# Performance work log

Hardware: AMD Instinct MI355X
Metric: run time of the kernel (lower is better)

The kernel has to match this reference:

```python
import jax, jax.numpy as jnp
import numpy as np


def setup_inputs() -> dict:
    key = jax.random.key(0)
    k1, k2, k3, k4 = jax.random.split(key, 4)
    B, T_dec, T_enc, H2 = 8, 64, 512, 512  # H2 = 2*hiddenSize
    encoderOutput = jax.random.normal(k1, (B, T_enc, H2), dtype=jnp.float32)
    decoderInput = jax.random.normal(k2, (B, T_dec, H2), dtype=jnp.float32)
    # fc: Linear(4H -> 2H); torch weight layout [out, in] = [2H, 4H]
    W = jax.random.normal(k3, (H2, 2 * H2), dtype=jnp.float32) * (1.0 / np.sqrt(2 * H2))
    b = jax.random.normal(k4, (H2,), dtype=jnp.float32) * 0.01
    return {"encoderOutput": encoderOutput, "decoderInput": decoderInput, "W": W, "b": b}


def reference(encoderOutput, decoderInput, W, b):
    # Original: for each (i, j), fc(cat(dec[:,i], enc[:,j])) then log_softmax over
    # the FEATURE dim (dim=1 of the flattened [-1, 2H] tensor), then
    # context[:, i] = sum_j log_softmax(...) * enc[:, j].
    H2 = encoderOutput.shape[-1]
    W_dec = W[:, :H2]   # columns multiplying the decoder half of the concat
    W_enc = W[:, H2:]   # columns multiplying the encoder half
    dec_part = jnp.einsum('bid,od->bio', decoderInput, W_dec)   # [B, T_dec, 2H]
    enc_part = jnp.einsum('bjd,od->bjo', encoderOutput, W_enc)  # [B, T_enc, 2H]
    logits = dec_part[:, :, None, :] + enc_part[:, None, :, :] + b  # [B, T_dec, T_enc, 2H]
    alpha = jax.nn.log_softmax(logits, axis=-1)  # softmax over feature dim, as in source
    context = jnp.einsum('bijd,bjd->bid', alpha, encoderOutput)  # [B, T_dec, 2H]
    return context
```

## Files before the change

### kernel.cpp

```cpp
#include <hip/hip_runtime.h>


namespace {
constexpr int kH  = 512;
constexpr int kTD = 64;
constexpr int kTE = 512;
constexpr int kB  = 8;
constexpr int kRD = kB * kTD;
constexpr int kRE = kB * kTE;
constexpr int kRT = kRD + kRE;
}

typedef __attribute__((ext_vector_type(8))) short short8;
typedef __attribute__((ext_vector_type(4))) float floatx4;

__device__ __forceinline__ unsigned short f2bf(float x) {
    unsigned u = __float_as_uint(x);
    u += 0x7fffu + ((u >> 16) & 1u);
    return (unsigned short)(u >> 16);
}
__device__ __forceinline__ float bf2f(unsigned short h) {
    return __uint_as_float(((unsigned)h) << 16);
}

__global__ __launch_bounds__(256) void cast_misc(
    const float* __restrict__ W, const float* __restrict__ dec,
    unsigned short* __restrict__ Wd, unsigned short* __restrict__ We,
    unsigned short* __restrict__ dec_bf,
    float* __restrict__ S1, float* __restrict__ S2)
{
    const int idx = blockIdx.x * 256 + threadIdx.x;
    const int row = idx >> 10, col = idx & 1023;
    const unsigned short v = f2bf(W[idx]);
    if (col < kH) Wd[row * kH + col] = v;
    else          We[row * kH + (col - kH)] = v;
    if (idx < kRD * kH) dec_bf[idx] = f2bf(dec[idx]);
    if (idx < kB * kH) { S1[idx] = 0.f; S2[idx] = 0.f; }
}

__global__ __launch_bounds__(256) void cast_enc(
    const float* __restrict__ enc, unsigned short* __restrict__ enc_bf)
{
    const int idx = blockIdx.x * 256 + threadIdx.x;
    const float4 v = ((const float4*)enc)[idx];
    ushort4 o;
    o.x = f2bf(v.x); o.y = f2bf(v.y); o.z = f2bf(v.z); o.w = f2bf(v.w);
    ((ushort4*)enc_bf)[idx] = o;
}

__global__ __launch_bounds__(64) void gemm1(
    const unsigned short* __restrict__ enc_bf,
    const unsigned short* __restrict__ dec_bf,
    const unsigned short* __restrict__ Wd,
    const unsigned short* __restrict__ We,
    const float* __restrict__ bias,
    unsigned short* __restrict__ part_bf, unsigned short* __restrict__ uv)
{
    const int tile = blockIdx.x;
    const int ns = tile & 7, ms = tile >> 3;
    const int l = threadIdx.x;
    const int lr = l & 15, lq = l >> 4;
    const bool isenc = (ms >= 8);
    const unsigned short* A = isenc ? (enc_bf + (size_t)(ms - 8) * 64 * kH)
                                    : (dec_bf + (size_t)ms * 64 * kH);
    const unsigned short* Bw = isenc ? We : Wd;
    const unsigned short* a0 = A + (size_t)lr * kH + lq * 8;
    const unsigned short* b0 = Bw + (size_t)(ns * 64 + lr) * kH + lq * 8;

    floatx4 acc[4][4];
#pragma unroll
    for (int m = 0; m < 4; ++m)
#pragma unroll
        for (int n = 0; n < 4; ++n) acc[m][n] = (floatx4){0.f, 0.f, 0.f, 0.f};

    for (int k0 = 0; k0 < kH; k0 += 32) {
        short8 af[4], bf[4];
#pragma unroll
        for (int m = 0; m < 4; ++m) af[m] = *(const short8*)(a0 + (size_t)m * 16 * kH + k0);
#pragma unroll
        for (int n = 0; n < 4; ++n) bf[n] = *(const short8*)(b0 + (size_t)n * 16 * kH + k0);
#pragma unroll
        for (int m = 0; m < 4; ++m)
#pragma unroll
            for (int n = 0; n < 4; ++n)
                acc[m][n] = __builtin_amdgcn_mfma_f32_16x16x32_bf16(af[m], bf[n], acc[m][n], 0, 0, 0);
    }

    const int rowbase = ms * 64, colbase = ns * 64;
#pragma unroll
    for (int n = 0; n < 4; ++n) {
        const int col = colbase + n * 16 + lr;
        const float bv = isenc ? bias[col] : 0.f;
#pragma unroll
        for (int m = 0; m < 4; ++m) {
            const int row0 = rowbase + m * 16 + lq * 4;
#pragma unroll
            for (int r = 0; r < 4; ++r) {
                const float v = acc[m][n][r];
                const size_t off = (size_t)(row0 + r) * kH + col;
                part_bf[off] = f2bf(v);
                uv[off]      = f2bf(__expf(v + bv));
            }
        }
    }
}

__global__ __launch_bounds__(256) void transpose_enc(
    const float* __restrict__ enc, unsigned short* __restrict__ encT)
{
    __shared__ unsigned short s[32][33];
    const int b = blockIdx.z, j0 = blockIdx.y * 32, d0 = blockIdx.x * 32;
    const int tx = threadIdx.x & 31, ty = threadIdx.x >> 5;
    const float* src = enc + ((size_t)b * kTE + j0) * kH + d0;
#pragma unroll
    for (int jj = 0; jj < 32; jj += 8)
        s[ty + jj][tx] = f2bf(src[(size_t)(ty + jj) * kH + tx]);
    __syncthreads();
    unsigned short* dst = encT + ((size_t)b * kH + d0) * kTE + j0;
#pragma unroll
    for (int dd = 0; dd < 32; dd += 8)
        dst[(size_t)(ty + dd) * kTE + tx] = s[tx][ty + dd];
}

__global__ __launch_bounds__(256) void s1s2_k(
    const float* __restrict__ enc, const unsigned short* __restrict__ part_bf,
    float* __restrict__ S1, float* __restrict__ S2)
{
    const int d = blockIdx.x * 256 + threadIdx.x;
    const int b = blockIdx.y, jc = blockIdx.z;
    const float* e = enc + ((size_t)b * kTE + jc * 32) * kH + d;
    const unsigned short* p = part_bf + (size_t)(kRD + b * kTE + jc * 32) * kH + d;
    float s1 = 0.f, s2 = 0.f;
#pragma unroll 4
    for (int j = 0; j < 32; ++j) {
        const float ev = e[(size_t)j * kH];
        const float pv = bf2f(p[(size_t)j * kH]);
        s1 += ev;
        s2 = fmaf(pv, ev, s2);
    }
    atomicAdd(&S1[b * kH + d], s1);
    atomicAdd(&S2[b * kH + d], s2);
}

__global__ __launch_bounds__(64) void pgemm_lse(
    const unsigned short* __restrict__ uv, unsigned short* __restrict__ lse_bf)
{
    const int w = blockIdx.x;
    const int b = w >> 7, rem = w & 127;
    const int it = rem >> 5, jt = rem & 31;
    const int l = threadIdx.x;
    const int lr = l & 15, lq = l >> 4;
    const unsigned short* ua = uv + (size_t)(b * 64 + it * 16 + lr) * kH + lq * 8;
    const unsigned short* vb = uv + (size_t)(kRD + b * kTE + jt * 16 + lr) * kH + lq * 8;

    floatx4 acc = (floatx4){0.f, 0.f, 0.f, 0.f};
    for (int k0 = 0; k0 < kH; k0 += 32)
        acc = __builtin_amdgcn_mfma_f32_16x16x32_bf16(
            *(const short8*)(ua + k0), *(const short8*)(vb + k0), acc, 0, 0, 0);

    const int jcol = jt * 16 + lr;
#pragma unroll
    for (int r = 0; r < 4; ++r) {
        const int i = it * 16 + lq * 4 + r;
        lse_bf[(size_t)(b * kTD + i) * kTE + jcol] = f2bf(__logf(acc[r]));
    }
}

__global__ __launch_bounds__(64) void final_k(
    const unsigned short* __restrict__ lse_bf,
    const unsigned short* __restrict__ encT,
    const unsigned short* __restrict__ part_bf,
    const float* __restrict__ bias,
    const float* __restrict__ S1, const float* __restrict__ S2,
    float* __restrict__ out)
{
    const int w = blockIdx.x;
    const int b = w >> 7, rem = w & 127;
    const int it = rem >> 5, dt = rem & 31;
    const int l = threadIdx.x;
    const int lr = l & 15, lq = l >> 4;
    const unsigned short* la = lse_bf + (size_t)(b * kTD + it * 16 + lr) * kTE + lq * 8;
    const unsigned short* eb = encT + ((size_t)b * kH + dt * 16 + lr) * kTE + lq * 8;

    floatx4 acc = (floatx4){0.f, 0.f, 0.f, 0.f};
    for (int k0 = 0; k0 < kTE; k0 += 32)
        acc = __builtin_amdgcn_mfma_f32_16x16x32_bf16(
            *(const short8*)(la + k0), *(const short8*)(eb + k0), acc, 0, 0, 0);

    const int d = dt * 16 + lr;
    const float s1 = S1[b * kH + d], s2 = S2[b * kH + d], bv = bias[d];
#pragma unroll
    for (int r = 0; r < 4; ++r) {
        const int i = it * 16 + lq * 4 + r;
        const float dp = bf2f(part_bf[(size_t)(b * kTD + i) * kH + d]);
        out[(size_t)(b * kTD + i) * kH + d] = fmaf(dp + bv, s1, s2) - acc[r];
    }
}

extern "C" void kernel_launch(void* const* d_in, const int* in_sizes, int n_in,
                              void* d_out, int out_size, void* d_ws, size_t ws_size,
                              hipStream_t stream)
{
    (void)in_sizes; (void)n_in; (void)out_size; (void)ws_size;
    const float* enc  = (const float*)d_in[0];
    const float* dec  = (const float*)d_in[1];
    const float* W    = (const float*)d_in[2];
    const float* bias = (const float*)d_in[3];
    float* out = (float*)d_out;

    char* base = (char*)d_ws;
    unsigned short* part_bf = (unsigned short*)(base);
    unsigned short* uv      = (unsigned short*)(base + 4718592);
    unsigned short* encX    = (unsigned short*)(base + 9437184);
    unsigned short* dec_bf  = (unsigned short*)(base + 13631488);
    unsigned short* Wd      = (unsigned short*)(base + 14155776);
    unsigned short* We      = (unsigned short*)(base + 14680064);
    unsigned short* lse_bf  = (unsigned short*)(base + 15204352);
    float*          S1      = (float*)(base + 15728640);
    float*          S2      = (float*)(base + 15745024);

    cast_misc<<<2048, 256, 0, stream>>>(W, dec, Wd, We, dec_bf, S1, S2);
    cast_enc<<<2048, 256, 0, stream>>>(enc, encX);
    gemm1<<<576, 64, 0, stream>>>(encX, dec_bf, Wd, We, bias, part_bf, uv);
    transpose_enc<<<dim3(16, 16, 8), 256, 0, stream>>>(enc, encX);
    s1s2_k<<<dim3(2, 8, 16), 256, 0, stream>>>(enc, part_bf, S1, S2);
    pgemm_lse<<<1024, 64, 0, stream>>>(uv, lse_bf);
    final_k<<<1024, 64, 0, stream>>>(lse_bf, encX, part_bf, bias, S1, S2, out);
}
```

Measured before the change: 108.0 us.

## Fuse casts, transpose, and reductions; split-K GEMMs across four waves

Merges the weight/decoder cast, encoder cast and encoder transpose into one kernel, and merges the LSE pgemm with the S1/S2 reduction into one launch. This cuts the launch count from seven to four. gemm1 and the two small GEMMs move from single-wave 64-thread blocks to 256-thread blocks: gemm1 gives each wave a quadrant of the tile, while the LSE and final GEMMs split K across four waves and reduce through LDS with vectorized epilogues. The intent is fewer launches and better latency hiding per block. The cost is extra LDS reduction work, a __syncthreads per block, and fewer blocks in the final GEMM.

```diff
diff --git a/kernel.cpp b/kernel.cpp
--- a/kernel.cpp
+++ b/kernel.cpp
@@ -8,7 +8,6 @@
 constexpr int kB  = 8;
 constexpr int kRD = kB * kTD;
 constexpr int kRE = kB * kTE;
-constexpr int kRT = kRD + kRE;
 }
 
 typedef __attribute__((ext_vector_type(8))) short short8;
@@ -23,32 +22,46 @@
     return __uint_as_float(((unsigned)h) << 16);
 }
 
-__global__ __launch_bounds__(256) void cast_misc(
+__global__ __launch_bounds__(256) void fused_cast(
     const float* __restrict__ W, const float* __restrict__ dec,
+    const float* __restrict__ enc,
     unsigned short* __restrict__ Wd, unsigned short* __restrict__ We,
     unsigned short* __restrict__ dec_bf,
+    unsigned short* __restrict__ enc_bf, unsigned short* __restrict__ encT,
     float* __restrict__ S1, float* __restrict__ S2)
 {
-    const int idx = blockIdx.x * 256 + threadIdx.x;
-    const int row = idx >> 10, col = idx & 1023;
-    const unsigned short v = f2bf(W[idx]);
-    if (col < kH) Wd[row * kH + col] = v;
-    else          We[row * kH + (col - kH)] = v;
-    if (idx < kRD * kH) dec_bf[idx] = f2bf(dec[idx]);
-    if (idx < kB * kH) { S1[idx] = 0.f; S2[idx] = 0.f; }
-}
-
-__global__ __launch_bounds__(256) void cast_enc(
-    const float* __restrict__ enc, unsigned short* __restrict__ enc_bf)
-{
-    const int idx = blockIdx.x * 256 + threadIdx.x;
-    const float4 v = ((const float4*)enc)[idx];
-    ushort4 o;
-    o.x = f2bf(v.x); o.y = f2bf(v.y); o.z = f2bf(v.z); o.w = f2bf(v.w);
-    ((ushort4*)enc_bf)[idx] = o;
-}
-
-__global__ __launch_bounds__(64) void gemm1(
+    const int blk = blockIdx.x, t = threadIdx.x;
+    if (blk < 2048) {
+        const int idx = blk * 256 + t;
+        const int row = idx >> 10, col = idx & 1023;
+        const unsigned short v = f2bf(W[idx]);
+        if (col < kH) Wd[row * kH + col] = v;
+        else          We[row * kH + (col - kH)] = v;
+        if (idx < kRD * kH) dec_bf[idx] = f2bf(dec[idx]);
+        if (idx < kB * kH) { S1[idx] = 0.f; S2[idx] = 0.f; }
+    } else {
+        __shared__ unsigned short s[32][33];
+        const int tid = blk - 2048;
+        const int b = tid >> 8, rem = tid & 255;
+        const int j0 = (rem >> 4) * 32, d0 = (rem & 15) * 32;
+        const int tx = t & 31, ty = t >> 5;
+        const float* src = enc + ((size_t)b * kTE + j0) * kH + d0;
+        unsigned short* edst = enc_bf + ((size_t)b * kTE + j0) * kH + d0;
+#pragma unroll
+        for (int jj = 0; jj < 32; jj += 8) {
+            const unsigned short h = f2bf(src[(size_t)(ty + jj) * kH + tx]);
+            s[ty + jj][tx] = h;
+            edst[(size_t)(ty + jj) * kH + tx] = h;
+        }
+        __syncthreads();
+        unsigned short* tdst = encT + ((size_t)b * kH + d0) * kTE + j0;
+#pragma unroll
+        for (int dd = 0; dd < 32; dd += 8)
+            tdst[(size_t)(ty + dd) * kTE + tx] = s[tx][ty + dd];
+    }
+}
+
+__global__ __launch_bounds__(256) void gemm1(
     const unsigned short* __restrict__ enc_bf,
     const unsigned short* __restrict__ dec_bf,
     const unsigned short* __restrict__ Wd,
@@ -58,41 +71,42 @@
 {
     const int tile = blockIdx.x;
     const int ns = tile & 7, ms = tile >> 3;
-    const int l = threadIdx.x;
+    const int t = threadIdx.x, w = t >> 6, l = t & 63;
+    const int qm = w >> 1, qn = w & 1;
     const int lr = l & 15, lq = l >> 4;
     const bool isenc = (ms >= 8);
     const unsigned short* A = isenc ? (enc_bf + (size_t)(ms - 8) * 64 * kH)
                                     : (dec_bf + (size_t)ms * 64 * kH);
     const unsigned short* Bw = isenc ? We : Wd;
-    const unsigned short* a0 = A + (size_t)lr * kH + lq * 8;
-    const unsigned short* b0 = Bw + (size_t)(ns * 64 + lr) * kH + lq * 8;
-
-    floatx4 acc[4][4];
-#pragma unroll
-    for (int m = 0; m < 4; ++m)
-#pragma unroll
-        for (int n = 0; n < 4; ++n) acc[m][n] = (floatx4){0.f, 0.f, 0.f, 0.f};
+    const unsigned short* a0 = A + (size_t)(qm * 32 + lr) * kH + lq * 8;
+    const unsigned short* b0 = Bw + (size_t)(ns * 64 + qn * 32 + lr) * kH + lq * 8;
+
+    floatx4 acc[2][2];
+#pragma unroll
+    for (int m = 0; m < 2; ++m)
+#pragma unroll
+        for (int n = 0; n < 2; ++n) acc[m][n] = (floatx4){0.f, 0.f, 0.f, 0.f};
 
     for (int k0 = 0; k0 < kH; k0 += 32) {
-        short8 af[4], bf[4];
-#pragma unroll
-        for (int m = 0; m < 4; ++m) af[m] = *(const short8*)(a0 + (size_t)m * 16 * kH + k0);
-#pragma unroll
-        for (int n = 0; n < 4; ++n) bf[n] = *(const short8*)(b0 + (size_t)n * 16 * kH + k0);
-#pragma unroll
-        for (int m = 0; m < 4; ++m)
-#pragma unroll
-            for (int n = 0; n < 4; ++n)
+        short8 af[2], bf[2];
+#pragma unroll
+        for (int m = 0; m < 2; ++m) af[m] = *(const short8*)(a0 + (size_t)m * 16 * kH + k0);
+#pragma unroll
+        for (int n = 0; n < 2; ++n) bf[n] = *(const short8*)(b0 + (size_t)n * 16 * kH + k0);
+#pragma unroll
+        for (int m = 0; m < 2; ++m)
+#pragma unroll
+            for (int n = 0; n < 2; ++n)
                 acc[m][n] = __builtin_amdgcn_mfma_f32_16x16x32_bf16(af[m], bf[n], acc[m][n], 0, 0, 0);
     }
 
-    const int rowbase = ms * 64, colbase = ns * 64;
-#pragma unroll
-    for (int n = 0; n < 4; ++n) {
+    const int rowbase = ms * 64 + qm * 32, colbase = ns * 64 + qn * 32;
+#pragma unroll
+    for (int n = 0; n < 2; ++n) {
         const int col = colbase + n * 16 + lr;
         const float bv = isenc ? bias[col] : 0.f;
 #pragma unroll
-        for (int m = 0; m < 4; ++m) {
+        for (int m = 0; m < 2; ++m) {
             const int row0 = rowbase + m * 16 + lq * 4;
 #pragma unroll
             for (int r = 0; r < 4; ++r) {
@@ -105,68 +119,69 @@
     }
 }
 
-__global__ __launch_bounds__(256) void transpose_enc(
-    const float* __restrict__ enc, unsigned short* __restrict__ encT)
-{
-    __shared__ unsigned short s[32][33];
-    const int b = blockIdx.z, j0 = blockIdx.y * 32, d0 = blockIdx.x * 32;
-    const int tx = threadIdx.x & 31, ty = threadIdx.x >> 5;
-    const float* src = enc + ((size_t)b * kTE + j0) * kH + d0;
-#pragma unroll
-    for (int jj = 0; jj < 32; jj += 8)
-        s[ty + jj][tx] = f2bf(src[(size_t)(ty + jj) * kH + tx]);
-    __syncthreads();
-    unsigned short* dst = encT + ((size_t)b * kH + d0) * kTE + j0;
-#pragma unroll
-    for (int dd = 0; dd < 32; dd += 8)
-        dst[(size_t)(ty + dd) * kTE + tx] = s[tx][ty + dd];
-}
-
-__global__ __launch_bounds__(256) void s1s2_k(
+__global__ __launch_bounds__(256) void lse_s1s2(
+    const unsigned short* __restrict__ uv, unsigned short* __restrict__ lse_bf,
     const float* __restrict__ enc, const unsigned short* __restrict__ part_bf,
     float* __restrict__ S1, float* __restrict__ S2)
 {
-    const int d = blockIdx.x * 256 + threadIdx.x;
-    const int b = blockIdx.y, jc = blockIdx.z;
-    const float* e = enc + ((size_t)b * kTE + jc * 32) * kH + d;
-    const unsigned short* p = part_bf + (size_t)(kRD + b * kTE + jc * 32) * kH + d;
-    float s1 = 0.f, s2 = 0.f;
+    __shared__ float red[4][16][68];
+    const int blk = blockIdx.x, t = threadIdx.x;
+    if (blk < 256) {
+        const int b = blk >> 5, rem = blk & 31;
+        const int it = rem >> 3, jt = rem & 7;
+        const int w = t >> 6, l = t & 63;
+        const int lr = l & 15, lq = l >> 4;
+        const unsigned short* ua = uv + (size_t)(b * 64 + it * 16 + lr) * kH + w * 128 + lq * 8;
+        const unsigned short* vb = uv + (size_t)(kRD + b * kTE + jt * 64 + lr) * kH + w * 128 + lq * 8;
+
+        floatx4 acc[4];
+#pragma unroll
+        for (int n = 0; n < 4; ++n) acc[n] = (floatx4){0.f, 0.f, 0.f, 0.f};
+#pragma unroll
+        for (int k0 = 0; k0 < 128; k0 += 32) {
+            const short8 af = *(const short8*)(ua + k0);
+#pragma unroll
+            for (int n = 0; n < 4; ++n)
+                acc[n] = __builtin_amdgcn_mfma_f32_16x16x32_bf16(
+                    af, *(const short8*)(vb + (size_t)n * 16 * kH + k0), acc[n], 0, 0, 0);
+        }
+#pragma unroll
+        for (int n = 0; n < 4; ++n)
+#pragma unroll
+            for (int r = 0; r < 4; ++r)
+                red[w][lq * 4 + r][n * 16 + lr] = acc[n][r];
+        __syncthreads();
+        const int i = t >> 4, j0 = (t & 15) * 4;
+        float4 s = *(const float4*)&red[0][i][j0];
+        const float4 s1 = *(const float4*)&red[1][i][j0];
+        const float4 s2 = *(const float4*)&red[2][i][j0];
+        const float4 s3 = *(const float4*)&red[3][i][j0];
+        s.x += s1.x + s2.x + s3.x; s.y += s1.y + s2.y + s3.y;
+        s.z += s1.z + s2.z + s3.z; s.w += s1.w + s2.w + s3.w;
+        ushort4 o;
+        o.x = f2bf(__logf(s.x)); o.y = f2bf(__logf(s.y));
+        o.z = f2bf(__logf(s.z)); o.w = f2bf(__logf(s.w));
+        *(ushort4*)(lse_bf + (size_t)(b * kTD + it * 16 + i) * kTE + jt * 64 + j0) = o;
+    } else {
+        const int blk2 = blk - 256;
+        const int jc = blk2 & 15, b = (blk2 >> 4) & 7, dh = blk2 >> 7;
+        const int d = dh * 256 + t;
+        const float* e = enc + ((size_t)b * kTE + jc * 32) * kH + d;
+        const unsigned short* p = part_bf + (size_t)(kRD + b * kTE + jc * 32) * kH + d;
+        float s1 = 0.f, s2 = 0.f;
 #pragma unroll 4
-    for (int j = 0; j < 32; ++j) {
-        const float ev = e[(size_t)j * kH];
-        const float pv = bf2f(p[(size_t)j * kH]);
-        s1 += ev;
-        s2 = fmaf(pv, ev, s2);
-    }
-    atomicAdd(&S1[b * kH + d], s1);
-    atomicAdd(&S2[b * kH + d], s2);
-}
-
-__global__ __launch_bounds__(64) void pgemm_lse(
-    const unsigned short* __restrict__ uv, unsigned short* __restrict__ lse_bf)
-{
-    const int w = blockIdx.x;
-    const int b = w >> 7, rem = w & 127;
-    const int it = rem >> 5, jt = rem & 31;
-    const int l = threadIdx.x;
-    const int lr = l & 15, lq = l >> 4;
-    const unsigned short* ua = uv + (size_t)(b * 64 + it * 16 + lr) * kH + lq * 8;
-    const unsigned short* vb = uv + (size_t)(kRD + b * kTE + jt * 16 + lr) * kH + lq * 8;
-
-    floatx4 acc = (floatx4){0.f, 0.f, 0.f, 0.f};
-    for (int k0 = 0; k0 < kH; k0 += 32)
-        acc = __builtin_amdgcn_mfma_f32_16x16x32_bf16(
-            *(const short8*)(ua + k0), *(const short8*)(vb + k0), acc, 0, 0, 0);
-
-    const int jcol = jt * 16 + lr;
-#pragma unroll
-    for (int r = 0; r < 4; ++r) {
-        const int i = it * 16 + lq * 4 + r;
-        lse_bf[(size_t)(b * kTD + i) * kTE + jcol] = f2bf(__logf(acc[r]));
-    }
-}
-
-__global__ __launch_bounds__(64) void final_k(
+        for (int j = 0; j < 32; ++j) {
+            const float ev = e[(size_t)j * kH];
+            const float pv = bf2f(p[(size_t)j * kH]);
+            s1 += ev;
+            s2 = fmaf(pv, ev, s2);
+        }
+        atomicAdd(&S1[b * kH + d], s1);
+        atomicAdd(&S2[b * kH + d], s2);
+    }
+}
+
+__global__ __launch_bounds__(256) void final_k(
     const unsigned short* __restrict__ lse_bf,
     const unsigned short* __restrict__ encT,
     const unsigned short* __restrict__ part_bf,
@@ -174,27 +189,52 @@
     const float* __restrict__ S1, const float* __restrict__ S2,
     float* __restrict__ out)
 {
-    const int w = blockIdx.x;
-    const int b = w >> 7, rem = w & 127;
-    const int it = rem >> 5, dt = rem & 31;
-    const int l = threadIdx.x;
+    __shared__ float red[4][16][68];
+    const int blk = blockIdx.x, t = threadIdx.x;
+    const int b = blk >> 5, rem = blk & 31;
+    const int it = rem >> 3, dt = rem & 7;
+    const int w = t >> 6, l = t & 63;
     const int lr = l & 15, lq = l >> 4;
-    const unsigned short* la = lse_bf + (size_t)(b * kTD + it * 16 + lr) * kTE + lq * 8;
-    const unsigned short* eb = encT + ((size_t)b * kH + dt * 16 + lr) * kTE + lq * 8;
-
-    floatx4 acc = (floatx4){0.f, 0.f, 0.f, 0.f};
-    for (int k0 = 0; k0 < kTE; k0 += 32)
-        acc = __builtin_amdgcn_mfma_f32_16x16x32_bf16(
-            *(const short8*)(la + k0), *(const short8*)(eb + k0), acc, 0, 0, 0);
-
-    const int d = dt * 16 + lr;
-    const float s1 = S1[b * kH + d], s2 = S2[b * kH + d], bv = bias[d];
-#pragma unroll
-    for (int r = 0; r < 4; ++r) {
-        const int i = it * 16 + lq * 4 + r;
-        const float dp = bf2f(part_bf[(size_t)(b * kTD + i) * kH + d]);
-        out[(size_t)(b * kTD + i) * kH + d] = fmaf(dp + bv, s1, s2) - acc[r];
-    }
+    const unsigned short* la = lse_bf + (size_t)(b * kTD + it * 16 + lr) * kTE + w * 128 + lq * 8;
+    const unsigned short* eb = encT + ((size_t)b * kH + dt * 64 + lr) * kTE + w * 128 + lq * 8;
+
+    floatx4 acc[4];
+#pragma unroll
+    for (int n = 0; n < 4; ++n) acc[n] = (floatx4){0.f, 0.f, 0.f, 0.f};
+#pragma unroll
+    for (int k0 = 0; k0 < 128; k0 += 32) {
+        const short8 af = *(const short8*)(la + k0);
+#pragma unroll
+        for (int n = 0; n < 4; ++n)
+            acc[n] = __builtin_amdgcn_mfma_f32_16x16x32_bf16(
+                af, *(const short8*)(eb + (size_t)n * 16 * kTE + k0), acc[n], 0, 0, 0);
+    }
+#pragma unroll
+    for (int n = 0; n < 4; ++n)
+#pragma unroll
+        for (int r = 0; r < 4; ++r)
+            red[w][lq * 4 + r][n * 16 + lr] = acc[n][r];
+    __syncthreads();
+    const int i = t >> 4, d0 = (t & 15) * 4;
+    float4 m = *(const float4*)&red[0][i][d0];
+    const float4 m1 = *(const float4*)&red[1][i][d0];
+    const float4 m2 = *(const float4*)&red[2][i][d0];
+    const float4 m3 = *(const float4*)&red[3][i][d0];
+    m.x += m1.x + m2.x + m3.x; m.y += m1.y + m2.y + m3.y;
+    m.z += m1.z + m2.z + m3.z; m.w += m1.w + m2.w + m3.w;
+
+    const int gd = dt * 64 + d0;
+    const float4 s1 = *(const float4*)(S1 + b * kH + gd);
+    const float4 s2 = *(const float4*)(S2 + b * kH + gd);
+    const float4 bi = *(const float4*)(bias + gd);
+    const int row = b * kTD + it * 16 + i;
+    const ushort4 dp = *(const ushort4*)(part_bf + (size_t)row * kH + gd);
+    float4 o;
+    o.x = fmaf(bf2f(dp.x) + bi.x, s1.x, s2.x) - m.x;
+    o.y = fmaf(bf2f(dp.y) + bi.y, s1.y, s2.y) - m.y;
+    o.z = fmaf(bf2f(dp.z) + bi.z, s1.z, s2.z) - m.z;
+    o.w = fmaf(bf2f(dp.w) + bi.w, s1.w, s2.w) - m.w;
+    *(float4*)(out + (size_t)row * kH + gd) = o;
 }
 
 extern "C" void kernel_launch(void* const* d_in, const int* in_sizes, int n_in,
@@ -211,19 +251,18 @@
     char* base = (char*)d_ws;
     unsigned short* part_bf = (unsigned short*)(base);
     unsigned short* uv      = (unsigned short*)(base + 4718592);
-    unsigned short* encX    = (unsigned short*)(base + 9437184);
-    unsigned short* dec_bf  = (unsigned short*)(base + 13631488);
-    unsigned short* Wd      = (unsigned short*)(base + 14155776);
-    unsigned short* We      = (unsigned short*)(base + 14680064);
-    unsigned short* lse_bf  = (unsigned short*)(base + 15204352);
-    float*          S1      = (float*)(base + 15728640);
-    float*          S2      = (float*)(base + 15745024);
-
-    cast_misc<<<2048, 256, 0, stream>>>(W, dec, Wd, We, dec_bf, S1, S2);
-    cast_enc<<<2048, 256, 0, stream>>>(enc, encX);
-    gemm1<<<576, 64, 0, stream>>>(encX, dec_bf, Wd, We, bias, part_bf, uv);
-    transpose_enc<<<dim3(16, 16, 8), 256, 0, stream>>>(enc, encX);
-    s1s2_k<<<dim3(2, 8, 16), 256, 0, stream>>>(enc, part_bf, S1, S2);
-    pgemm_lse<<<1024, 64, 0, stream>>>(uv, lse_bf);
-    final_k<<<1024, 64, 0, stream>>>(lse_bf, encX, part_bf, bias, S1, S2, out);
-}
+    unsigned short* enc_bf  = (unsigned short*)(base + 9437184);
+    unsigned short* encT    = (unsigned short*)(base + 13631488);
+    unsigned short* dec_bf  = (unsigned short*)(base + 17825792);
+    unsigned short* Wd      = (unsigned short*)(base + 18350080);
+    unsigned short* We      = (unsigned short*)(base + 18874368);
+    unsigned short* lse_bf  = (unsigned short*)(base + 19398656);
+    float*          S1      = (float*)(base + 19922944);
+    float*          S2      = (float*)(base + 19939328);
+
+    fused_cast<<<4096, 256, 0, stream>>>(W, dec, enc, Wd, We, dec_bf,
+                                         enc_bf, encT, S1, S2);
+    gemm1<<<576, 256, 0, stream>>>(enc_bf, dec_bf, Wd, We, bias, part_bf, uv);
+    lse_s1s2<<<512, 256, 0, stream>>>(uv, lse_bf, enc, part_bf, S1, S2);
+    final_k<<<256, 256, 0, stream>>>(lse_bf, encT, part_bf, bias, S1, S2, out);
+}
```

After: 102.7 us. 4.9% less time.
